# Optimization experiments

Measured on AMD Instinct MI355X. Metric: run time of the kernel, lower is better.

## Reference

```python
import jax, jax.numpy as jnp
import numpy as np

K = 2        # kernel_size
DIL = 1      # dilation
H = 768      # h_size = nhid + nout
NOUT = 256
NLAYER = 10  # weight-tied iterations of f_theta


def conv1d(x, w, b, dilation=1):
    # x: (B, Cin, L), w: (Cout, Cin, K) -> (B, Cout, L-(K-1)*dilation)
    y = jax.lax.conv_general_dilated(
        x, w, window_strides=(1,), padding='VALID',
        rhs_dilation=(dilation,), dimension_numbers=('NCH', 'OIH', 'NCH'))
    return y + b[None, :, None]


def setup_inputs() -> dict:
    key = jax.random.key(0)
    ks = jax.random.split(key, 5)
    B, NINP, L = 4, 512, 1024
    bound = 0.01  # init_weights() uses N(0, 0.01)
    return {
        'X': jax.random.normal(ks[0], (B, NINP, L), dtype=jnp.float32),
        'z0': jnp.zeros((B, 2 * H, 1), dtype=jnp.float32),
        'inject_w': bound * jax.random.normal(ks[1], (4 * H, NINP, K), dtype=jnp.float32),
        'inject_b': bound * jax.random.normal(ks[2], (4 * H,), dtype=jnp.float32),
        'conv_w': bound * jax.random.normal(ks[3], (4 * H, H, K), dtype=jnp.float32),
        'conv_b': bound * jax.random.normal(ks[4], (4 * H,), dtype=jnp.float32),
    }


def reference(X, z0, inject_w, inject_b, conv_w, conv_b):
    B, _, L = X.shape
    pad_in = K - 1            # inject conv causal padding
    pad_h = (K - 1) * DIL     # hidden conv causal padding

    # us = inject_conv(pad(X)) : (B, 4H, L), computed once
    Xp = jnp.pad(X, ((0, 0), (0, 0), (pad_in, 0)))
    us = conv1d(Xp, inject_w, inject_b, dilation=1)

    z0h, z0c = z0[:, :H], z0[:, H:]  # (B, H, 1) each
    hid_pad = jnp.broadcast_to(z0h, (B, H, pad_h))  # repeat history into padding

    def step(z1s, _):
        z1h, z1c = z1s[:, :H], z1s[:, H:]
        # shifted cell state: cat([z0c, z1c])[:, :, :-1]
        z0c_s = jnp.concatenate([z0c, z1c[:, :, :-1]], axis=2)
        # weight-tied causal dilated conv on hidden part, history in padding
        xh = jnp.concatenate([hid_pad, z1h], axis=2)
        out = us + conv1d(xh, conv_w, conv_b, dilation=DIL)  # (B, 4H, L)
        it, ot, gt, ft = jnp.split(out, 4, axis=1)
        ct = jax.nn.sigmoid(ft) * z0c_s + jax.nn.sigmoid(it) * jnp.tanh(gt)
        ht = jax.nn.sigmoid(ot) * jnp.tanh(ct)
        return jnp.concatenate([ht, ct], axis=1), None

    z1s0 = jnp.zeros((B, 2 * H, L), dtype=X.dtype)
    z1s, _ = jax.lax.scan(step, z1s0, None, length=NLAYER)

    out = jnp.transpose(z1s[:, H - NOUT:H], (0, 2, 1))  # (B, L, nout)
    z0_out = z1s[:, :, -1:]                              # history repackaging
    return out, z0_out
```

## Files before the change

### kernel.cpp

```cpp
#include <hip/hip_runtime.h>
#include <hip/hip_bf16.h>
#include <stdint.h>


#define B_    4
#define L_    1024
#define LP1   1025
#define H_    768
#define NG_   3072
#define NINP_ 512
#define NOUT_ 256

typedef __bf16 bf16x8 __attribute__((ext_vector_type(8)));
typedef float f32x4 __attribute__((ext_vector_type(4)));
using bf16_t = __hip_bfloat16;

__device__ __forceinline__ float sigf(float x){ return 1.f/(1.f + __expf(-x)); }
__device__ __forceinline__ float tanhf_(float x){
  float e = __expf(-2.f*fabsf(x));
  float r = (1.f - e)/(1.f + e);
  return x >= 0.f ? r : -r;
}

__device__ __forceinline__ void gl_lds16(const void* g, void* l){
  __builtin_amdgcn_global_load_lds(
    (const __attribute__((address_space(1))) uint32_t*)g,
    (__attribute__((address_space(3))) uint32_t*)l, 16, 0, 0);
}

__global__ void init_k(const float* __restrict__ z0, bf16_t* __restrict__ Xt,
                       bf16_t* __restrict__ Hb0, bf16_t* __restrict__ Hb1,
                       float* __restrict__ Cb0, float* __restrict__ Cb1){
  int tid = blockIdx.x*256 + threadIdx.x;
  if (tid < B_*NINP_){
    int b = tid >> 9, i = tid & 511;
    Xt[(size_t)b*LP1*NINP_ + i] = __float2bfloat16(0.f);
  }
  if (tid < B_*H_){
    int b = tid / H_, j = tid % H_;
    size_t idx = (size_t)b*LP1*H_ + j;
    bf16_t hz = __float2bfloat16(z0[b*2*H_ + j]);
    float  cz = z0[b*2*H_ + H_ + j];
    Hb0[idx] = hz; Hb1[idx] = hz; Cb0[idx] = cz; Cb1[idx] = cz;
  }
}

__global__ void prep_w(const float* __restrict__ iw, const float* __restrict__ ib,
                       const float* __restrict__ cw, const float* __restrict__ cb,
                       bf16_t* __restrict__ Wit, bf16_t* __restrict__ Wct,
                       float* __restrict__ bias){
  int op = blockIdx.x;
  int gate = (op >> 4) & 3;
  int j = ((op >> 6) << 4) | (op & 15);
  int o = gate*H_ + j;
  const float2* s2 = (const float2*)(iw + (size_t)o*NINP_*2);
  bf16_t* d = Wit + (size_t)op*(2*NINP_);
  for (int i = threadIdx.x; i < NINP_; i += 256){
    float2 v = s2[i];
    d[i]        = __float2bfloat16(v.x);
    d[NINP_ + i]= __float2bfloat16(v.y);
  }
  const float2* c2 = (const float2*)(cw + (size_t)o*H_*2);
  bf16_t* dc = Wct + (size_t)op*(2*H_);
  for (int i = threadIdx.x; i < H_; i += 256){
    float2 v = c2[i];
    dc[i]      = __float2bfloat16(v.x);
    dc[H_ + i] = __float2bfloat16(v.y);
  }
  if (threadIdx.x == 0) bias[op] = ib[o] + cb[o];
}

__global__ void transpose_x(const float* __restrict__ X, bf16_t* __restrict__ Xt){
  __shared__ float tile[64][65];
  int b = blockIdx.z;
  int t0 = blockIdx.x*64, i0 = blockIdx.y*64;
  int c = threadIdx.x & 63;
  for (int r = threadIdx.x >> 6; r < 64; r += 4)
    tile[r][c] = X[((size_t)b*NINP_ + i0 + r)*L_ + t0 + c];
  __syncthreads();
  for (int r = threadIdx.x >> 6; r < 64; r += 4)
    Xt[((size_t)b*LP1 + t0 + r + 1)*NINP_ + i0 + c] = __float2bfloat16(tile[c][r]);
}

template<int KTOT, int AROW, int MODE>
__launch_bounds__(256, 2)
__global__ void gemm_fused(const bf16_t* __restrict__ A, const bf16_t* __restrict__ Bt,
                           const float* __restrict__ bias, float* __restrict__ usOut,
                           const float* __restrict__ usIn, const float* __restrict__ Cprev,
                           float* __restrict__ Cnew, bf16_t* __restrict__ Hnew){
  __shared__ bf16_t As[128*32];
  __shared__ bf16_t Bs[128*32];
  const int tid = threadIdx.x;
  const int l = tid & 63;
  const int w = tid >> 6;
  const int wm = w >> 1, wn = w & 1;
  const int bm0 = blockIdx.x * 128;
  const int bn0 = blockIdx.y * 128;

  f32x4 acc[4][4];
#pragma unroll
  for (int i = 0; i < 4; ++i)
#pragma unroll
    for (int jj = 0; jj < 4; ++jj)
      acc[i][jj] = (f32x4){0.f,0.f,0.f,0.f};

  const int sr = l >> 2;
  const int sb = (l & 3) << 4;
  const char* ag[2]; const char* bg[2];
  char* al[2]; char* bl[2];
#pragma unroll
  for (int n = 0; n < 2; ++n){
    const int r = w*16 + n*64 + sr;
    const int m = bm0 + r;
    const int b = m >> 10, t = m & 1023;
    ag[n] = (const char*)A + ((size_t)(b*LP1 + t)*AROW)*2 + sb;
    bg[n] = (const char*)Bt + ((size_t)(bn0 + r)*KTOT)*2 + sb;
    al[n] = (char*)As + (w + n*4)*1024;
    bl[n] = (char*)Bs + (w + n*4)*1024;
  }

  const int kg = (l >> 4) << 4;
  const int lr = l & 15;

  for (int kt = 0; kt < KTOT/32; ++kt){
    const int ko = kt << 6;
    gl_lds16(ag[0] + ko, al[0]);
    gl_lds16(ag[1] + ko, al[1]);
    gl_lds16(bg[0] + ko, bl[0]);
    gl_lds16(bg[1] + ko, bl[1]);
    __syncthreads();
    bf16x8 af[4], bfv[4];
#pragma unroll
    for (int f = 0; f < 4; ++f){
      af[f]  = *reinterpret_cast<const bf16x8*>((const char*)As + (wm*64 + f*16 + lr)*64 + kg);
      bfv[f] = *reinterpret_cast<const bf16x8*>((const char*)Bs + (wn*64 + f*16 + lr)*64 + kg);
    }
#pragma unroll
    for (int fm = 0; fm < 4; ++fm)
#pragma unroll
      for (int fn = 0; fn < 4; ++fn)
        acc[fm][fn] = __builtin_amdgcn_mfma_f32_16x16x32_bf16(af[fm], bfv[fn], acc[fm][fn], 0, 0, 0);
    __syncthreads();
  }

  if (MODE == 0){
#pragma unroll
    for (int fm = 0; fm < 4; ++fm){
      const int mbase = bm0 + wm*64 + fm*16 + ((l >> 4) << 2);
#pragma unroll
      for (int fn = 0; fn < 4; ++fn){
        const int op = bn0 + wn*64 + fn*16 + lr;
        const float bz = bias[op];
#pragma unroll
        for (int r = 0; r < 4; ++r)
          usOut[(size_t)(mbase + r)*NG_ + op] = acc[fm][fn][r] + bz;
      }
    }
  } else {
    const int jblk = (bn0 + wn*64) >> 6;
    const int j = jblk*16 + lr;
#pragma unroll
    for (int fm = 0; fm < 4; ++fm){
      const int mbase = bm0 + wm*64 + fm*16 + ((l >> 4) << 2);
#pragma unroll
      for (int r = 0; r < 4; ++r){
        const int m = mbase + r;
        const int b = m >> 10, t = m & 1023;
        const float* ur = usIn + (size_t)m*NG_ + jblk*64 + lr;
        const float ig = acc[fm][0][r] + ur[0];
        const float og = acc[fm][1][r] + ur[16];
        const float gg = acc[fm][2][r] + ur[32];
        const float fg = acc[fm][3][r] + ur[48];
        const size_t base = (size_t)(b*LP1 + t)*H_ + j;
        const float cp = Cprev[base];
        const float c  = sigf(fg)*cp + sigf(ig)*tanhf_(gg);
        const float h  = sigf(og)*tanhf_(c);
        Cnew[base + H_] = c;
        Hnew[base + H_] = __float2bfloat16(h);
      }
    }
  }
}

__global__ void iter0_k(const float* __restrict__ us, bf16_t* __restrict__ Hn,
                        float* __restrict__ Cn){
  const int m = blockIdx.y;
  const int j = blockIdx.x*256 + threadIdx.x;
  const int b = m >> 10, t = m & 1023;
  const int opb = ((j >> 4) << 6) | (j & 15);
  const float* ur = us + (size_t)m*NG_ + opb;
  const float ig = ur[0], og = ur[16], gg = ur[32];
  const float c = sigf(ig)*tanhf_(gg);
  const float h = sigf(og)*tanhf_(c);
  const size_t idx = (size_t)(b*LP1 + t + 1)*H_ + j;
  Cn[idx] = c;
  Hn[idx] = __float2bfloat16(h);
}

__global__ void finalize_k(const bf16_t* __restrict__ Hf, const float* __restrict__ Cf,
                           float* __restrict__ out){
  const int tid = blockIdx.x*256 + threadIdx.x;
  if (tid < B_*L_*NOUT_){
    const int n = tid & 255, t = (tid >> 8) & 1023, b = tid >> 18;
    out[tid] = __bfloat162float(Hf[((size_t)b*LP1 + t + 1)*H_ + (H_ - NOUT_) + n]);
  } else if (tid < B_*L_*NOUT_ + B_*2*H_){
    const int r = tid - B_*L_*NOUT_;
    const int b = r / (2*H_), ch = r % (2*H_);
    const size_t row = ((size_t)b*LP1 + L_)*H_;
    out[tid] = (ch < H_) ? __bfloat162float(Hf[row + ch]) : Cf[row + (ch - H_)];
  }
}

extern "C" void kernel_launch(void* const* d_in, const int* in_sizes, int n_in,
                              void* d_out, int out_size, void* d_ws, size_t ws_size,
                              hipStream_t stream){
  const float* X   = (const float*)d_in[0];
  const float* z0  = (const float*)d_in[1];
  const float* iw  = (const float*)d_in[2];
  const float* ib  = (const float*)d_in[3];
  const float* cw  = (const float*)d_in[4];
  const float* cbv = (const float*)d_in[5];
  float* out = (float*)d_out;

  char* ws = (char*)d_ws;
  float*  us   = (float*) (ws + 0);
  bf16_t* Xt   = (bf16_t*)(ws + 50331648);
  bf16_t* Wit  = (bf16_t*)(ws + 54530048);
  bf16_t* Wct  = (bf16_t*)(ws + 60821504);
  float*  bias = (float*) (ws + 70258688);
  bf16_t* Hb0  = (bf16_t*)(ws + 70270976);
  bf16_t* Hb1  = (bf16_t*)(ws + 76568576);
  float*  Cb0  = (float*) (ws + 82866176);
  float*  Cb1  = (float*) (ws + 95461376);

  init_k<<<12, 256, 0, stream>>>(z0, Xt, Hb0, Hb1, Cb0, Cb1);
  prep_w<<<NG_, 256, 0, stream>>>(iw, ib, cw, cbv, Wit, Wct, bias);
  transpose_x<<<dim3(L_/64, NINP_/64, B_), 256, 0, stream>>>(X, Xt);

  gemm_fused<1024, NINP_, 0><<<dim3(32, 24), 256, 0, stream>>>(
      Xt, Wit, bias, us, nullptr, nullptr, nullptr, nullptr);

  iter0_k<<<dim3(3, 4096), 256, 0, stream>>>(us, Hb0, Cb0);

  bf16_t* Hp = Hb0; float* Cp = Cb0;
  bf16_t* Hn = Hb1; float* Cn = Cb1;
  for (int it = 1; it <= 9; ++it){
    gemm_fused<1536, H_, 1><<<dim3(32, 24), 256, 0, stream>>>(
        Hp, Wct, nullptr, nullptr, us, Cp, Cn, Hn);
    bf16_t* th = Hp; Hp = Hn; Hn = th;
    float*  tc = Cp; Cp = Cn; Cn = tc;
  }

  finalize_k<<<(B_*L_*NOUT_ + B_*2*H_ + 255)/256, 256, 0, stream>>>(Hp, Cp, out);
}
```

Before: 623.5 us.

## Store gate preactivations and cell state in fp16, prune last iteration to needed outputs

Stores the injected preactivations as packed fp16x4 per hidden unit and the cell state in fp16, which halves the memory traffic of the epilogue loads. It also swizzles the workgroup order and raises the occupancy hint to 3. The final iteration computes only the last 256 hidden channels plus a small tail kernel for the final timestep's state, skipping unused work. The risks are lost precision in the fp16 storage and register pressure from the higher occupancy bound.

```diff
diff --git a/kernel.cpp b/kernel.cpp
--- a/kernel.cpp
+++ b/kernel.cpp
@@ -13,6 +13,7 @@
 
 typedef __bf16 bf16x8 __attribute__((ext_vector_type(8)));
 typedef float f32x4 __attribute__((ext_vector_type(4)));
+typedef _Float16 f16x4 __attribute__((ext_vector_type(4)));
 using bf16_t = __hip_bfloat16;
 
 __device__ __forceinline__ float sigf(float x){ return 1.f/(1.f + __expf(-x)); }
@@ -30,7 +31,7 @@
 
 __global__ void init_k(const float* __restrict__ z0, bf16_t* __restrict__ Xt,
                        bf16_t* __restrict__ Hb0, bf16_t* __restrict__ Hb1,
-                       float* __restrict__ Cb0, float* __restrict__ Cb1){
+                       _Float16* __restrict__ Cb0, _Float16* __restrict__ Cb1){
   int tid = blockIdx.x*256 + threadIdx.x;
   if (tid < B_*NINP_){
     int b = tid >> 9, i = tid & 511;
@@ -40,7 +41,7 @@
     int b = tid / H_, j = tid % H_;
     size_t idx = (size_t)b*LP1*H_ + j;
     bf16_t hz = __float2bfloat16(z0[b*2*H_ + j]);
-    float  cz = z0[b*2*H_ + H_ + j];
+    _Float16 cz = (_Float16)z0[b*2*H_ + H_ + j];
     Hb0[idx] = hz; Hb1[idx] = hz; Cb0[idx] = cz; Cb1[idx] = cz;
   }
 }
@@ -48,7 +49,7 @@
 __global__ void prep_w(const float* __restrict__ iw, const float* __restrict__ ib,
                        const float* __restrict__ cw, const float* __restrict__ cb,
                        bf16_t* __restrict__ Wit, bf16_t* __restrict__ Wct,
-                       float* __restrict__ bias){
+                       float* __restrict__ bias4){
   int op = blockIdx.x;
   int gate = (op >> 4) & 3;
   int j = ((op >> 6) << 4) | (op & 15);
@@ -57,8 +58,8 @@
   bf16_t* d = Wit + (size_t)op*(2*NINP_);
   for (int i = threadIdx.x; i < NINP_; i += 256){
     float2 v = s2[i];
-    d[i]        = __float2bfloat16(v.x);
-    d[NINP_ + i]= __float2bfloat16(v.y);
+    d[i]         = __float2bfloat16(v.x);
+    d[NINP_ + i] = __float2bfloat16(v.y);
   }
   const float2* c2 = (const float2*)(cw + (size_t)o*H_*2);
   bf16_t* dc = Wct + (size_t)op*(2*H_);
@@ -67,7 +68,7 @@
     dc[i]      = __float2bfloat16(v.x);
     dc[H_ + i] = __float2bfloat16(v.y);
   }
-  if (threadIdx.x == 0) bias[op] = ib[o] + cb[o];
+  if (threadIdx.x == 0) bias4[j*4 + gate] = ib[o] + cb[o];
 }
 
 __global__ void transpose_x(const float* __restrict__ X, bf16_t* __restrict__ Xt){
@@ -83,19 +84,23 @@
 }
 
 template<int KTOT, int AROW, int MODE>
-__launch_bounds__(256, 2)
+__launch_bounds__(256, 3)
 __global__ void gemm_fused(const bf16_t* __restrict__ A, const bf16_t* __restrict__ Bt,
-                           const float* __restrict__ bias, float* __restrict__ usOut,
-                           const float* __restrict__ usIn, const float* __restrict__ Cprev,
-                           float* __restrict__ Cnew, bf16_t* __restrict__ Hnew){
+                           const float* __restrict__ bias4, f16x4* __restrict__ us4,
+                           const _Float16* __restrict__ Cprev, _Float16* __restrict__ Cnew,
+                           bf16_t* __restrict__ Hnew, int bn_base){
   __shared__ bf16_t As[128*32];
   __shared__ bf16_t Bs[128*32];
   const int tid = threadIdx.x;
   const int l = tid & 63;
   const int w = tid >> 6;
   const int wm = w >> 1, wn = w & 1;
-  const int bm0 = blockIdx.x * 128;
-  const int bn0 = blockIdx.y * 128;
+
+  const int nwg = gridDim.x * gridDim.y;
+  int flat = blockIdx.y * gridDim.x + blockIdx.x;
+  flat = (flat & 7) * (nwg >> 3) + (flat >> 3);
+  const int bm0 = (flat & 31) * 128;
+  const int bn0 = bn_base + (flat >> 5) * 128;
 
   f32x4 acc[4][4];
 #pragma unroll
@@ -143,72 +148,101 @@
     __syncthreads();
   }
 
+  const int jblk = (bn0 + wn*64) >> 6;
+  const int j = jblk*16 + lr;
+  const int rq = (l >> 4) << 2;
+
   if (MODE == 0){
+    const float4 bz = ((const float4*)bias4)[j];
 #pragma unroll
     for (int fm = 0; fm < 4; ++fm){
-      const int mbase = bm0 + wm*64 + fm*16 + ((l >> 4) << 2);
-#pragma unroll
-      for (int fn = 0; fn < 4; ++fn){
-        const int op = bn0 + wn*64 + fn*16 + lr;
-        const float bz = bias[op];
-#pragma unroll
-        for (int r = 0; r < 4; ++r)
-          usOut[(size_t)(mbase + r)*NG_ + op] = acc[fm][fn][r] + bz;
+      const int mbase = bm0 + wm*64 + fm*16 + rq;
+#pragma unroll
+      for (int r = 0; r < 4; ++r){
+        const int m = mbase + r;
+        f16x4 v = { (_Float16)(acc[fm][0][r] + bz.x), (_Float16)(acc[fm][1][r] + bz.y),
+                    (_Float16)(acc[fm][2][r] + bz.z), (_Float16)(acc[fm][3][r] + bz.w) };
+        us4[(size_t)m*H_ + j] = v;
       }
     }
   } else {
-    const int jblk = (bn0 + wn*64) >> 6;
-    const int j = jblk*16 + lr;
 #pragma unroll
     for (int fm = 0; fm < 4; ++fm){
-      const int mbase = bm0 + wm*64 + fm*16 + ((l >> 4) << 2);
+      const int mbase = bm0 + wm*64 + fm*16 + rq;
+      f16x4 uv[4]; _Float16 cp16[4]; size_t hcb[4];
 #pragma unroll
       for (int r = 0; r < 4; ++r){
         const int m = mbase + r;
         const int b = m >> 10, t = m & 1023;
-        const float* ur = usIn + (size_t)m*NG_ + jblk*64 + lr;
-        const float ig = acc[fm][0][r] + ur[0];
-        const float og = acc[fm][1][r] + ur[16];
-        const float gg = acc[fm][2][r] + ur[32];
-        const float fg = acc[fm][3][r] + ur[48];
-        const size_t base = (size_t)(b*LP1 + t)*H_ + j;
-        const float cp = Cprev[base];
-        const float c  = sigf(fg)*cp + sigf(ig)*tanhf_(gg);
+        uv[r] = us4[(size_t)m*H_ + j];
+        hcb[r] = (size_t)(b*LP1 + t)*H_ + j;
+        cp16[r] = Cprev[hcb[r]];
+      }
+#pragma unroll
+      for (int r = 0; r < 4; ++r){
+        const float ig = acc[fm][0][r] + (float)uv[r][0];
+        const float og = acc[fm][1][r] + (float)uv[r][1];
+        const float gg = acc[fm][2][r] + (float)uv[r][2];
+        const float fg = acc[fm][3][r] + (float)uv[r][3];
+        const float c  = sigf(fg)*(float)cp16[r] + sigf(ig)*tanhf_(gg);
         const float h  = sigf(og)*tanhf_(c);
-        Cnew[base + H_] = c;
-        Hnew[base + H_] = __float2bfloat16(h);
+        Cnew[hcb[r] + H_] = (_Float16)c;
+        Hnew[hcb[r] + H_] = __float2bfloat16(h);
       }
     }
   }
 }
 
-__global__ void iter0_k(const float* __restrict__ us, bf16_t* __restrict__ Hn,
-                        float* __restrict__ Cn){
+__global__ void iter0_k(const f16x4* __restrict__ us4, bf16_t* __restrict__ Hn,
+                        _Float16* __restrict__ Cn){
   const int m = blockIdx.y;
   const int j = blockIdx.x*256 + threadIdx.x;
   const int b = m >> 10, t = m & 1023;
-  const int opb = ((j >> 4) << 6) | (j & 15);
-  const float* ur = us + (size_t)m*NG_ + opb;
-  const float ig = ur[0], og = ur[16], gg = ur[32];
-  const float c = sigf(ig)*tanhf_(gg);
+  f16x4 u = us4[(size_t)m*H_ + j];
+  const float ig = (float)u[0], og = (float)u[1], gg = (float)u[2], fg = (float)u[3];
+  float cp = (t == 0) ? (float)Cn[(size_t)b*LP1*H_ + j] : 0.f;
+  const float c = sigf(fg)*cp + sigf(ig)*tanhf_(gg);
   const float h = sigf(og)*tanhf_(c);
   const size_t idx = (size_t)(b*LP1 + t + 1)*H_ + j;
-  Cn[idx] = c;
+  Cn[idx] = (_Float16)c;
   Hn[idx] = __float2bfloat16(h);
 }
 
-__global__ void finalize_k(const bf16_t* __restrict__ Hf, const float* __restrict__ Cf,
-                           float* __restrict__ out){
+__global__ void tail_k(const bf16_t* __restrict__ H8, const _Float16* __restrict__ C8,
+                       const f16x4* __restrict__ us4, const bf16_t* __restrict__ Wct,
+                       float* __restrict__ out){
+  const int b = blockIdx.y;
+  const int op = blockIdx.x*256 + threadIdx.x;
+  const int gate = (op >> 4) & 3, lr = op & 15;
+  const int j = ((op >> 6) << 4) | lr;
+  const bf16_t* a  = H8 + (size_t)(b*LP1 + 1023)*H_;
+  const bf16_t* wr = Wct + (size_t)op*1536;
+  float s = 0.f;
+#pragma unroll 4
+  for (int k2 = 0; k2 < 1536; k2 += 8){
+    bf16x8 av = *reinterpret_cast<const bf16x8*>(a + k2);
+    bf16x8 wv = *reinterpret_cast<const bf16x8*>(wr + k2);
+#pragma unroll
+    for (int u = 0; u < 8; ++u) s += (float)av[u]*(float)wv[u];
+  }
+  s += (float)us4[(size_t)(b*1024 + 1023)*H_ + j][gate];
+  const float si = __shfl(s, lr);
+  const float so = __shfl(s, lr + 16);
+  const float sg = __shfl(s, lr + 32);
+  const float sf = __shfl(s, lr + 48);
+  if (gate == 0){
+    const float cp = (float)C8[(size_t)(b*LP1 + 1023)*H_ + j];
+    const float c = sigf(sf)*cp + sigf(si)*tanhf_(sg);
+    const float h = sigf(so)*tanhf_(c);
+    out[B_*L_*NOUT_ + b*2*H_ + j]      = h;
+    out[B_*L_*NOUT_ + b*2*H_ + H_ + j] = c;
+  }
+}
+
+__global__ void finalize_k(const bf16_t* __restrict__ Hf, float* __restrict__ out){
   const int tid = blockIdx.x*256 + threadIdx.x;
-  if (tid < B_*L_*NOUT_){
-    const int n = tid & 255, t = (tid >> 8) & 1023, b = tid >> 18;
-    out[tid] = __bfloat162float(Hf[((size_t)b*LP1 + t + 1)*H_ + (H_ - NOUT_) + n]);
-  } else if (tid < B_*L_*NOUT_ + B_*2*H_){
-    const int r = tid - B_*L_*NOUT_;
-    const int b = r / (2*H_), ch = r % (2*H_);
-    const size_t row = ((size_t)b*LP1 + L_)*H_;
-    out[tid] = (ch < H_) ? __bfloat162float(Hf[row + ch]) : Cf[row + (ch - H_)];
-  }
+  const int n = tid & 255, t = (tid >> 8) & 1023, b = tid >> 18;
+  out[tid] = __bfloat162float(Hf[((size_t)b*LP1 + t + 1)*H_ + (H_ - NOUT_) + n]);
 }
 
 extern "C" void kernel_launch(void* const* d_in, const int* in_sizes, int n_in,
@@ -223,33 +257,38 @@
   float* out = (float*)d_out;
 
   char* ws = (char*)d_ws;
-  float*  us   = (float*) (ws + 0);
-  bf16_t* Xt   = (bf16_t*)(ws + 50331648);
-  bf16_t* Wit  = (bf16_t*)(ws + 54530048);
-  bf16_t* Wct  = (bf16_t*)(ws + 60821504);
-  float*  bias = (float*) (ws + 70258688);
-  bf16_t* Hb0  = (bf16_t*)(ws + 70270976);
-  bf16_t* Hb1  = (bf16_t*)(ws + 76568576);
-  float*  Cb0  = (float*) (ws + 82866176);
-  float*  Cb1  = (float*) (ws + 95461376);
+  f16x4*    us4  = (f16x4*)   (ws + 0);
+  bf16_t*   Xt   = (bf16_t*)  (ws + 25165824);
+  bf16_t*   Wit  = (bf16_t*)  (ws + 29364224);
+  bf16_t*   Wct  = (bf16_t*)  (ws + 35655680);
+  float*    bias4= (float*)   (ws + 45092864);
+  bf16_t*   Hb0  = (bf16_t*)  (ws + 45105152);
+  bf16_t*   Hb1  = (bf16_t*)  (ws + 51402752);
+  _Float16* Cb0  = (_Float16*)(ws + 57700352);
+  _Float16* Cb1  = (_Float16*)(ws + 63997952);
 
   init_k<<<12, 256, 0, stream>>>(z0, Xt, Hb0, Hb1, Cb0, Cb1);
-  prep_w<<<NG_, 256, 0, stream>>>(iw, ib, cw, cbv, Wit, Wct, bias);
+  prep_w<<<NG_, 256, 0, stream>>>(iw, ib, cw, cbv, Wit, Wct, bias4);
   transpose_x<<<dim3(L_/64, NINP_/64, B_), 256, 0, stream>>>(X, Xt);
 
   gemm_fused<1024, NINP_, 0><<<dim3(32, 24), 256, 0, stream>>>(
-      Xt, Wit, bias, us, nullptr, nullptr, nullptr, nullptr);
-
-  iter0_k<<<dim3(3, 4096), 256, 0, stream>>>(us, Hb0, Cb0);
-
-  bf16_t* Hp = Hb0; float* Cp = Cb0;
-  bf16_t* Hn = Hb1; float* Cn = Cb1;
-  for (int it = 1; it <= 9; ++it){
+      Xt, Wit, bias4, us4, nullptr, nullptr, nullptr, 0);
+
+  iter0_k<<<dim3(3, 4096), 256, 0, stream>>>(us4, Hb0, Cb0);
+
+  bf16_t* Hp = Hb0; _Float16* Cp = Cb0;
+  bf16_t* Hn = Hb1; _Float16* Cn = Cb1;
+  for (int it = 1; it <= 8; ++it){
     gemm_fused<1536, H_, 1><<<dim3(32, 24), 256, 0, stream>>>(
-        Hp, Wct, nullptr, nullptr, us, Cp, Cn, Hn);
+        Hp, Wct, nullptr, us4, Cp, Cn, Hn, 0);
     bf16_t* th = Hp; Hp = Hn; Hn = th;
-    float*  tc = Cp; Cp = Cn; Cn = tc;
-  }
-
-  finalize_k<<<(B_*L_*NOUT_ + B_*2*H_ + 255)/256, 256, 0, stream>>>(Hp, Cp, out);
-}
+    _Float16* tc = Cp; Cp = Cn; Cn = tc;
+  }
+
+  tail_k<<<dim3(12, B_), 256, 0, stream>>>(Hp, Cp, us4, Wct, out);
+
+  gemm_fused<1536, H_, 1><<<dim3(32, 8), 256, 0, stream>>>(
+      Hp, Wct, nullptr, us4, Cp, Cn, Hn, 2048);
+
+  finalize_k<<<4096, 256, 0, stream>>>(Hn, out);
+}
```

New measurement: 628.2 us. No clear change (+0.8%).
